# Performance work log

Measured on AMD Instinct MI355X. Metric: run time of the kernel, lower is better.

The kernel has to match this reference:

```python
import jax, jax.numpy as jnp
import numpy as np

SIGMA = 0.1
SIG2 = SIGMA * SIGMA  # sigma^2


def _gauss_conv(x, y, b):
    # x: BxNxD, y: BxKxD, b: BxKxd -> BxNxd
    # K_ij = exp(-||x_i - y_j||^2 / (2 sigma^2)); out_i = sum_j K_ij b_j
    d2 = jnp.sum((x[:, :, None, :] - y[:, None, :, :]) ** 2, axis=-1)  # BxNxK
    K = jnp.exp(-d2 / (2.0 * SIG2))
    return jnp.einsum('bnk,bkd->bnd', K, b)


def _gauss_grad(p, x):
    # grad-of-kernel N-body sum (py=px=p, y=x as in grad_kernel(mom, pos)):
    # out_i = sum_j <p_i, p_j> * grad_{x_i} K(x_i, x_j)
    #       = sum_j <p_i, p_j> * K_ij * (-(x_i - x_j) / sigma^2)
    diff = x[:, :, None, :] - x[:, None, :, :]            # BxNxKxD
    d2 = jnp.sum(diff ** 2, axis=-1)                      # BxNxK
    K = jnp.exp(-d2 / (2.0 * SIG2))
    C = jnp.einsum('bnd,bkd->bnk', p, p)                  # <p_i, p_j>
    return jnp.einsum('bnk,bnkd->bnd', -(K * C) / SIG2, diff)


def setup_inputs() -> dict:
    key = jax.random.key(0)
    k1, k2 = jax.random.split(key)
    B, N, D = 1, 8192, 3
    mom = jax.random.normal(k1, (B, N, D), dtype=jnp.float32)
    pos = jax.random.normal(k2, (B, N, D), dtype=jnp.float32)
    return {"mom": mom, "pos": pos}


def reference(mom, pos):
    # variational_evolve: (dmom/dt, dpos/dt) = (-grad_kernel(mom,pos), kernel(pos,pos,mom))
    dmom = -_gauss_grad(mom, pos)
    dpos = _gauss_conv(pos, pos, mom)
    return (dmom, dpos)
```

## Files before the change

### kernel.cpp

```cpp
#include <hip/hip_runtime.h>


#define NPTS  8192
#define NCXY  16
#define NCZ   32
#define NCELL (NCXY * NCXY * NCZ)
#define ORIGIN    (-4.0f)
#define INV_EDGE  2.0f
#define INV_EDGEZ 4.0f
#define RCUT      0.5f

#define A_DOT 144.269504088896f
#define A_R   (-72.134752044448f)
#define INV_SIG2 100.0f

#define EXP2(x) __builtin_amdgcn_exp2f(x)

__device__ __forceinline__ int clampi(int c, int hi) { return min(max(c, 0), hi); }

__device__ __forceinline__ int cell_of(float x, float y, float z) {
    const int cx = clampi((int)floorf((x - ORIGIN) * INV_EDGE),  NCXY - 1);
    const int cy = clampi((int)floorf((y - ORIGIN) * INV_EDGE),  NCXY - 1);
    const int cz = clampi((int)floorf((z - ORIGIN) * INV_EDGEZ), NCZ  - 1);
    return (cx * NCXY + cy) * NCZ + cz;
}

__global__ __launch_bounds__(1024)
void k_countscan(const float* __restrict__ pos,
                 int* __restrict__ start, int* __restrict__ cur)
{
    __shared__ int cnt[NCELL];
    __shared__ int wtot[16];
    __shared__ int wexcl[16];
    const int t = threadIdx.x;
    const int lane = t & 63;
    const int wid = t >> 6;

    #pragma unroll
    for (int k = 0; k < NCELL / 1024; ++k) cnt[t + k * 1024] = 0;
    __syncthreads();

    #pragma unroll
    for (int k = 0; k < NPTS / 1024; ++k) {
        const int i = t + k * 1024;
        atomicAdd(&cnt[cell_of(pos[3*i+0], pos[3*i+1], pos[3*i+2])], 1);
    }
    __syncthreads();

    int pre[8];
    int s = 0;
    #pragma unroll
    for (int k = 0; k < 8; ++k) { pre[k] = s; s += cnt[8*t + k]; }
    int p = s;
    #pragma unroll
    for (int off = 1; off < 64; off <<= 1) {
        const int v = __shfl_up(p, off);
        if (lane >= off) p += v;
    }
    if (lane == 63) wtot[wid] = p;
    __syncthreads();
    if (t < 16) {
        const int w = wtot[t];
        int q = w;
        #pragma unroll
        for (int off = 1; off < 16; off <<= 1) {
            const int v = __shfl_up(q, off);
            if (t >= off) q += v;
        }
        wexcl[t] = q - w;
    }
    __syncthreads();
    const int base = wexcl[wid] + (p - s);
    #pragma unroll
    for (int k = 0; k < 8; ++k) {
        const int v = base + pre[k];
        start[8*t + k] = v;
        cur[8*t + k] = v;
    }
    if (t == 0) start[NCELL] = NPTS;
}

__global__ __launch_bounds__(256)
void k_scatter(const float* __restrict__ mom, const float* __restrict__ pos,
               int* __restrict__ cur,
               float* __restrict__ pmP, float* __restrict__ pmM,
               int* __restrict__ inv)
{
    const int i = blockIdx.x * 256 + threadIdx.x;
    const float x = pos[3*i+0], y = pos[3*i+1], z = pos[3*i+2];
    const int dst = atomicAdd(&cur[cell_of(x, y, z)], 1);
    const float r2 = x*x + y*y + z*z;
    reinterpret_cast<float4*>(pmP)[dst] = make_float4(A_DOT*x, A_DOT*y, A_DOT*z, A_R*r2);
    reinterpret_cast<float4*>(pmM)[dst] = make_float4(mom[3*i+0], mom[3*i+1], mom[3*i+2], 0.0f);
    inv[dst] = i;
}

__global__ __launch_bounds__(256)
void k_main(const float* __restrict__ mom, const float* __restrict__ pos,
            const float* __restrict__ pmP, const float* __restrict__ pmM,
            const int* __restrict__ inv, const int* __restrict__ start,
            float* __restrict__ out)
{
    const int wid  = (blockIdx.x * 256 + threadIdx.x) >> 6;
    const int lane = threadIdx.x & 63;

    const int oi = inv[wid];
    const float xi = pos[3*oi+0], yi = pos[3*oi+1], zi = pos[3*oi+2];
    const float pxi = mom[3*oi+0], pyi = mom[3*oi+1], pzi = mom[3*oi+2];
    const float ci  = A_R * (xi*xi + yi*yi + zi*zi);

    const int cx = clampi((int)floorf((xi - ORIGIN) * INV_EDGE), NCXY - 1);
    const int cy = clampi((int)floorf((yi - ORIGIN) * INV_EDGE), NCXY - 1);
    const int x0 = max(cx - 1, 0), x1 = min(cx + 1, NCXY - 1);
    const int y0 = max(cy - 1, 0), y1 = min(cy + 1, NCXY - 1);
    const int z0 = clampi((int)floorf((zi - RCUT - ORIGIN) * INV_EDGEZ), NCZ - 1);
    const int z1 = clampi((int)floorf((zi + RCUT - ORIGIN) * INV_EDGEZ), NCZ - 1);
    const int wy = y1 - y0 + 1;
    const int ncol = (x1 - x0 + 1) * wy;

    int st_l = 0, en_l = 0;
    if (lane < ncol) {
        const int nx = x0 + lane / wy;
        const int ny = y0 + lane % wy;
        const int base = (nx * NCXY + ny) * NCZ;
        st_l = start[base + z0];
        en_l = start[base + z1 + 1];
    }

    float S = 0.f, SPx = 0.f, SPy = 0.f, SPz = 0.f;
    float apx = 0.f, apy = 0.f, apz = 0.f;

    const float4* __restrict__ pmPv = reinterpret_cast<const float4*>(pmP);
    const float4* __restrict__ pmMv = reinterpret_cast<const float4*>(pmM);

    for (int p = 0; p < ncol; ++p) {
        const int st = __shfl(st_l, p);
        const int en = __shfl(en_l, p);
        for (int j = st + lane; j < en; j += 64) {
            const float4 P = pmPv[j];
            const float4 M = pmMv[j];
            float arg = __builtin_fmaf(zi, P.z, ci + P.w);
            arg = __builtin_fmaf(yi, P.y, arg);
            arg = __builtin_fmaf(xi, P.x, arg);
            const float K = EXP2(arg);
            const float C = __builtin_fmaf(pzi, M.z,
                              __builtin_fmaf(pyi, M.y, pxi * M.x));
            const float s = K * C;
            S += s;
            SPx = __builtin_fmaf(s, P.x, SPx);
            SPy = __builtin_fmaf(s, P.y, SPy);
            SPz = __builtin_fmaf(s, P.z, SPz);
            apx = __builtin_fmaf(K, M.x, apx);
            apy = __builtin_fmaf(K, M.y, apy);
            apz = __builtin_fmaf(K, M.z, apz);
        }
    }

    #pragma unroll
    for (int off = 1; off < 64; off <<= 1) {
        S   += __shfl_xor(S,   off);
        SPx += __shfl_xor(SPx, off);
        SPy += __shfl_xor(SPy, off);
        SPz += __shfl_xor(SPz, off);
        apx += __shfl_xor(apx, off);
        apy += __shfl_xor(apy, off);
        apz += __shfl_xor(apz, off);
    }

    if (lane == 0) {
        const float us = INV_SIG2 / A_DOT;
        out[3*oi+0] = INV_SIG2 * xi * S - us * SPx;
        out[3*oi+1] = INV_SIG2 * yi * S - us * SPy;
        out[3*oi+2] = INV_SIG2 * zi * S - us * SPz;
        out[3*NPTS + 3*oi+0] = apx;
        out[3*NPTS + 3*oi+1] = apy;
        out[3*NPTS + 3*oi+2] = apz;
    }
}

extern "C" void kernel_launch(void* const* d_in, const int* in_sizes, int n_in,
                              void* d_out, int out_size, void* d_ws, size_t ws_size,
                              hipStream_t stream)
{
    const float* mom = (const float*)d_in[0];
    const float* pos = (const float*)d_in[1];
    float* out = (float*)d_out;

    float* pmP  = (float*)d_ws;
    float* pmM  = pmP + (size_t)4 * NPTS;
    int* inv    = (int*)(pmM + (size_t)4 * NPTS);
    int* start  = inv + NPTS;
    int* cur    = start + NCELL + 1;

    k_countscan<<<1, 1024, 0, stream>>>(pos, start, cur);
    k_scatter<<<NPTS / 256, 256, 0, stream>>>(mom, pos, cur, pmP, pmM, inv);
    k_main<<<(NPTS * 64) / 256, 256, 0, stream>>>(mom, pos, pmP, pmM, inv, start, out);
}
```

Measured before the change: 24.86 us.

## Process two sorted targets per wave and tighten per-column z windows

Each wavefront now handles two neighbouring (cell-sorted) target points, so every loaded source pair (P, M) is evaluated against both targets, halving source memory traffic and loop overhead per interaction. Because the two targets' neighbourhoods can differ, the column range is widened to the union of both. Each column's z range is narrowed using the exact lateral distance from the target to the column, which skips cells outside the cutoff sphere. The cost is more registers, a possibly larger union window, and half as many waves for latency hiding.

```diff
diff --git a/kernel.cpp b/kernel.cpp
--- a/kernel.cpp
+++ b/kernel.cpp
@@ -6,9 +6,11 @@
 #define NCZ   32
 #define NCELL (NCXY * NCXY * NCZ)
 #define ORIGIN    (-4.0f)
+#define EDGE      0.5f
 #define INV_EDGE  2.0f
 #define INV_EDGEZ 4.0f
 #define RCUT      0.5f
+#define RCUT2     0.25f
 
 #define A_DOT 144.269504088896f
 #define A_R   (-72.134752044448f)
@@ -95,26 +97,66 @@
     inv[dst] = i;
 }
 
+__device__ __forceinline__ void eval_one(
+    const float4 P, const float4 M,
+    const float xi, const float yi, const float zi, const float ci,
+    const float pxi, const float pyi, const float pzi,
+    float& S, float& SPx, float& SPy, float& SPz,
+    float& apx, float& apy, float& apz)
+{
+    float arg = __builtin_fmaf(zi, P.z, ci + P.w);
+    arg = __builtin_fmaf(yi, P.y, arg);
+    arg = __builtin_fmaf(xi, P.x, arg);
+    const float K = EXP2(arg);
+    const float C = __builtin_fmaf(pzi, M.z, __builtin_fmaf(pyi, M.y, pxi * M.x));
+    const float s = K * C;
+    S += s;
+    SPx = __builtin_fmaf(s, P.x, SPx);
+    SPy = __builtin_fmaf(s, P.y, SPy);
+    SPz = __builtin_fmaf(s, P.z, SPz);
+    apx = __builtin_fmaf(K, M.x, apx);
+    apy = __builtin_fmaf(K, M.y, apy);
+    apz = __builtin_fmaf(K, M.z, apz);
+}
+
+__device__ __forceinline__ void zwin(float x, float y, float z,
+                                     float X0, float Y0, int& z0, int& z1)
+{
+    const float dx = fmaxf(fmaxf(X0 - x, x - (X0 + EDGE)), 0.0f);
+    const float dy = fmaxf(fmaxf(Y0 - y, y - (Y0 + EDGE)), 0.0f);
+    const float m2 = dx * dx + dy * dy;
+    if (m2 <= RCUT2) {
+        const float zr = __builtin_sqrtf(RCUT2 - m2);
+        z0 = clampi((int)floorf((z - zr - ORIGIN) * INV_EDGEZ), NCZ - 1);
+        z1 = clampi((int)floorf((z + zr - ORIGIN) * INV_EDGEZ), NCZ - 1);
+    } else {
+        z0 = 1; z1 = 0;
+    }
+}
+
 __global__ __launch_bounds__(256)
 void k_main(const float* __restrict__ mom, const float* __restrict__ pos,
             const float* __restrict__ pmP, const float* __restrict__ pmM,
             const int* __restrict__ inv, const int* __restrict__ start,
             float* __restrict__ out)
 {
-    const int wid  = (blockIdx.x * 256 + threadIdx.x) >> 6;
+    const int w    = (blockIdx.x * 256 + threadIdx.x) >> 6;
     const int lane = threadIdx.x & 63;
 
-    const int oi = inv[wid];
-    const float xi = pos[3*oi+0], yi = pos[3*oi+1], zi = pos[3*oi+2];
-    const float pxi = mom[3*oi+0], pyi = mom[3*oi+1], pzi = mom[3*oi+2];
-    const float ci  = A_R * (xi*xi + yi*yi + zi*zi);
-
-    const int cx = clampi((int)floorf((xi - ORIGIN) * INV_EDGE), NCXY - 1);
-    const int cy = clampi((int)floorf((yi - ORIGIN) * INV_EDGE), NCXY - 1);
-    const int x0 = max(cx - 1, 0), x1 = min(cx + 1, NCXY - 1);
-    const int y0 = max(cy - 1, 0), y1 = min(cy + 1, NCXY - 1);
-    const int z0 = clampi((int)floorf((zi - RCUT - ORIGIN) * INV_EDGEZ), NCZ - 1);
-    const int z1 = clampi((int)floorf((zi + RCUT - ORIGIN) * INV_EDGEZ), NCZ - 1);
+    const int oiA = inv[2*w], oiB = inv[2*w + 1];
+    const float xA = pos[3*oiA+0], yA = pos[3*oiA+1], zA = pos[3*oiA+2];
+    const float pxA = mom[3*oiA+0], pyA = mom[3*oiA+1], pzA = mom[3*oiA+2];
+    const float xB = pos[3*oiB+0], yB = pos[3*oiB+1], zB = pos[3*oiB+2];
+    const float pxB = mom[3*oiB+0], pyB = mom[3*oiB+1], pzB = mom[3*oiB+2];
+    const float cA = A_R * (xA*xA + yA*yA + zA*zA);
+    const float cB = A_R * (xB*xB + yB*yB + zB*zB);
+
+    const int cxA = clampi((int)floorf((xA - ORIGIN) * INV_EDGE), NCXY - 1);
+    const int cyA = clampi((int)floorf((yA - ORIGIN) * INV_EDGE), NCXY - 1);
+    const int cxB = clampi((int)floorf((xB - ORIGIN) * INV_EDGE), NCXY - 1);
+    const int cyB = clampi((int)floorf((yB - ORIGIN) * INV_EDGE), NCXY - 1);
+    const int x0 = max(min(cxA, cxB) - 1, 0), x1 = min(max(cxA, cxB) + 1, NCXY - 1);
+    const int y0 = max(min(cyA, cyB) - 1, 0), y1 = min(max(cyA, cyB) + 1, NCXY - 1);
     const int wy = y1 - y0 + 1;
     const int ncol = (x1 - x0 + 1) * wy;
 
@@ -122,13 +164,23 @@
     if (lane < ncol) {
         const int nx = x0 + lane / wy;
         const int ny = y0 + lane % wy;
-        const int base = (nx * NCXY + ny) * NCZ;
-        st_l = start[base + z0];
-        en_l = start[base + z1 + 1];
-    }
-
-    float S = 0.f, SPx = 0.f, SPy = 0.f, SPz = 0.f;
-    float apx = 0.f, apy = 0.f, apz = 0.f;
+        const float X0 = ORIGIN + nx * EDGE;
+        const float Y0 = ORIGIN + ny * EDGE;
+        int a0, a1, b0, b1;
+        zwin(xA, yA, zA, X0, Y0, a0, a1);
+        zwin(xB, yB, zB, X0, Y0, b0, b1);
+        int zlo = NCZ, zhi = -1;
+        if (a0 <= a1) { zlo = a0; zhi = a1; }
+        if (b0 <= b1) { zlo = min(zlo, b0); zhi = max(zhi, b1); }
+        if (zlo <= zhi) {
+            const int base = (nx * NCXY + ny) * NCZ;
+            st_l = start[base + zlo];
+            en_l = start[base + zhi + 1];
+        }
+    }
+
+    float SA=0.f, SPAx=0.f, SPAy=0.f, SPAz=0.f, apAx=0.f, apAy=0.f, apAz=0.f;
+    float SB=0.f, SPBx=0.f, SPBy=0.f, SPBz=0.f, apBx=0.f, apBy=0.f, apBz=0.f;
 
     const float4* __restrict__ pmPv = reinterpret_cast<const float4*>(pmP);
     const float4* __restrict__ pmMv = reinterpret_cast<const float4*>(pmM);
@@ -139,42 +191,46 @@
         for (int j = st + lane; j < en; j += 64) {
             const float4 P = pmPv[j];
             const float4 M = pmMv[j];
-            float arg = __builtin_fmaf(zi, P.z, ci + P.w);
-            arg = __builtin_fmaf(yi, P.y, arg);
-            arg = __builtin_fmaf(xi, P.x, arg);
-            const float K = EXP2(arg);
-            const float C = __builtin_fmaf(pzi, M.z,
-                              __builtin_fmaf(pyi, M.y, pxi * M.x));
-            const float s = K * C;
-            S += s;
-            SPx = __builtin_fmaf(s, P.x, SPx);
-            SPy = __builtin_fmaf(s, P.y, SPy);
-            SPz = __builtin_fmaf(s, P.z, SPz);
-            apx = __builtin_fmaf(K, M.x, apx);
-            apy = __builtin_fmaf(K, M.y, apy);
-            apz = __builtin_fmaf(K, M.z, apz);
+            eval_one(P, M, xA, yA, zA, cA, pxA, pyA, pzA,
+                     SA, SPAx, SPAy, SPAz, apAx, apAy, apAz);
+            eval_one(P, M, xB, yB, zB, cB, pxB, pyB, pzB,
+                     SB, SPBx, SPBy, SPBz, apBx, apBy, apBz);
         }
     }
 
     #pragma unroll
     for (int off = 1; off < 64; off <<= 1) {
-        S   += __shfl_xor(S,   off);
-        SPx += __shfl_xor(SPx, off);
-        SPy += __shfl_xor(SPy, off);
-        SPz += __shfl_xor(SPz, off);
-        apx += __shfl_xor(apx, off);
-        apy += __shfl_xor(apy, off);
-        apz += __shfl_xor(apz, off);
-    }
-
+        SA   += __shfl_xor(SA,   off);
+        SPAx += __shfl_xor(SPAx, off);
+        SPAy += __shfl_xor(SPAy, off);
+        SPAz += __shfl_xor(SPAz, off);
+        apAx += __shfl_xor(apAx, off);
+        apAy += __shfl_xor(apAy, off);
+        apAz += __shfl_xor(apAz, off);
+        SB   += __shfl_xor(SB,   off);
+        SPBx += __shfl_xor(SPBx, off);
+        SPBy += __shfl_xor(SPBy, off);
+        SPBz += __shfl_xor(SPBz, off);
+        apBx += __shfl_xor(apBx, off);
+        apBy += __shfl_xor(apBy, off);
+        apBz += __shfl_xor(apBz, off);
+    }
+
+    const float us = INV_SIG2 / A_DOT;
     if (lane == 0) {
-        const float us = INV_SIG2 / A_DOT;
-        out[3*oi+0] = INV_SIG2 * xi * S - us * SPx;
-        out[3*oi+1] = INV_SIG2 * yi * S - us * SPy;
-        out[3*oi+2] = INV_SIG2 * zi * S - us * SPz;
-        out[3*NPTS + 3*oi+0] = apx;
-        out[3*NPTS + 3*oi+1] = apy;
-        out[3*NPTS + 3*oi+2] = apz;
+        out[3*oiA+0] = INV_SIG2 * xA * SA - us * SPAx;
+        out[3*oiA+1] = INV_SIG2 * yA * SA - us * SPAy;
+        out[3*oiA+2] = INV_SIG2 * zA * SA - us * SPAz;
+        out[3*NPTS + 3*oiA+0] = apAx;
+        out[3*NPTS + 3*oiA+1] = apAy;
+        out[3*NPTS + 3*oiA+2] = apAz;
+    } else if (lane == 1) {
+        out[3*oiB+0] = INV_SIG2 * xB * SB - us * SPBx;
+        out[3*oiB+1] = INV_SIG2 * yB * SB - us * SPBy;
+        out[3*oiB+2] = INV_SIG2 * zB * SB - us * SPBz;
+        out[3*NPTS + 3*oiB+0] = apBx;
+        out[3*NPTS + 3*oiB+1] = apBy;
+        out[3*NPTS + 3*oiB+2] = apBz;
     }
 }
 
@@ -194,5 +250,5 @@
 
     k_countscan<<<1, 1024, 0, stream>>>(pos, start, cur);
     k_scatter<<<NPTS / 256, 256, 0, stream>>>(mom, pos, cur, pmP, pmM, inv);
-    k_main<<<(NPTS * 64) / 256, 256, 0, stream>>>(mom, pos, pmP, pmM, inv, start, out);
-}
+    k_main<<<(NPTS / 2 * 64) / 256, 256, 0, stream>>>(mom, pos, pmP, pmM, inv, start, out);
+}
```

After: 26.13 us. 5.1% more time.
